# Kernel tuning notes

Hardware: AMD Instinct MI355X
Metric: run time of the kernel (lower is better)

## Reference

```python
import jax, jax.numpy as jnp
import numpy as np

N = 8192
FEAT = 3
TRIG = 2
SA = 2
H = 64
ACT = 3
NEG = -1.0e9
EPS = 1e-5


def setup_inputs() -> dict:
    key = jax.random.key(0)
    ks = jax.random.split(key, 24)
    s = 0.05
    node_features = jax.random.uniform(ks[0], (N, FEAT), dtype=jnp.float32)
    adj = jax.random.randint(ks[1], (N, N), 0, 2).astype(jnp.float32)
    # ensure self-loops so every row has at least one neighbor
    adj_matrix = jnp.maximum(adj, jnp.eye(N, dtype=jnp.float32))
    trigger_context = jax.random.uniform(ks[2], (TRIG,), dtype=jnp.float32)
    sa_priors = jax.random.normal(ks[3], (N, SA), dtype=jnp.float32)
    p = lambda k, sh: jax.random.normal(k, sh, dtype=jnp.float32) * s
    return {
        "node_features": node_features,
        "adj_matrix": adj_matrix,
        "trigger_context": trigger_context,
        "sa_priors": sa_priors,
        # node_encoder: Linear(5,64) -> ReLU -> Linear(64,64)
        "w1": p(ks[4], (FEAT + TRIG, H)), "b1": jnp.zeros((H,), jnp.float32),
        "w2": p(ks[5], (H, H)), "b2": jnp.zeros((H,), jnp.float32),
        "wq": p(ks[6], (H, H)), "bq": jnp.zeros((H,), jnp.float32),
        "wk": p(ks[7], (H, H)), "bk": jnp.zeros((H,), jnp.float32),
        "wg": p(ks[8], (TRIG, H)), "bg": jnp.zeros((H,), jnp.float32),
        "stateful_bias": jnp.zeros((1,), jnp.float32),
        "wm": p(ks[9], (H, H)), "bm": jnp.zeros((H,), jnp.float32),
        "ln_g": jnp.ones((H,), jnp.float32), "ln_b": jnp.zeros((H,), jnp.float32),
        "wa1": p(ks[10], (H + SA, H)), "ba1": jnp.zeros((H,), jnp.float32),
        "wa2": p(ks[11], (H, ACT)), "ba2": jnp.zeros((ACT,), jnp.float32),
    }


def reference(node_features, adj_matrix, trigger_context, sa_priors,
              w1, b1, w2, b2, wq, bq, wk, bk, wg, bg, stateful_bias,
              wm, bm, ln_g, ln_b, wa1, ba1, wa2, ba2):
    n = node_features.shape[0]
    trig = jnp.broadcast_to(trigger_context[None, :], (n, TRIG))
    x = jnp.concatenate([node_features, trig], axis=1)          # [N, 5]
    h = jax.nn.relu(x @ w1 + b1) @ w2 + b2                       # [N, H]
    q = h @ wq + bq
    k = h @ wk + bk
    scores = (q @ k.T) * (1.0 / np.sqrt(H))                      # [N, N]
    gate_factor = jnp.mean(jax.nn.sigmoid(trigger_context @ wg + bg))
    topo = jnp.where(adj_matrix == 0, jnp.float32(NEG), adj_matrix)
    is_stateful = node_features[:, 2]
    is_reactive = 1.0 - trigger_context[0]
    sb = jnp.outer(is_stateful, is_stateful) * (stateful_bias[0] * is_reactive)
    scores = scores * gate_factor + topo + sb
    attn = jax.nn.softmax(scores, axis=1)                        # [N, N]
    messages = h @ wm + bm
    aggregated = attn @ messages                                 # [N, H]
    z = h + aggregated
    mu = jnp.mean(z, axis=-1, keepdims=True)
    var = jnp.mean(jnp.square(z - mu), axis=-1, keepdims=True)
    emb = (z - mu) * jax.lax.rsqrt(var + EPS) * ln_g + ln_b      # LayerNorm
    ai = jnp.concatenate([emb, sa_priors], axis=1)               # [N, H+2]
    q_values = jax.nn.relu(ai @ wa1 + ba1) @ wa2 + ba2           # [N, 3]
    return q_values
```

## Files before the change

### kernel.cpp

```cpp
#include <hip/hip_runtime.h>
#include <hip/hip_bf16.h>
#include <math.h>

#define N 8192
#define NEGV -1000000000.0f
#define EPSV 1e-05f
#define NSPLIT 8
#define CPS (N / NSPLIT)
#define NTILE (CPS / 64)

typedef short bf16x8 __attribute__((ext_vector_type(8)));
typedef float f32x4 __attribute__((ext_vector_type(4)));
typedef unsigned short u16;

#define WS_SCAL 0
#define WS_H    64
#define WS_ST   (WS_H + N * 64)
#define WS_SBI  (WS_ST + N)
#define WS_DEN  (WS_SBI + N)
#define WS_AGG  (WS_DEN + NSPLIT * N)
#define WS_F_END (WS_AGG + NSPLIT * N * 64)
#define WU_BASE (WS_F_END * 2)
#define WU_QB (WU_BASE)
#define WU_KB (WU_BASE + N * 64)
#define WU_MB (WU_BASE + 2 * N * 64)
#define WU_MT (WU_BASE + 3 * N * 64)

static __device__ __forceinline__ u16 f2bf(float f) {
    __hip_bfloat16 h = __float2bfloat16(f);
    return *(u16*)&h;
}

__global__ void prep_k(const float* __restrict__ tc, const float* __restrict__ wg,
                       const float* __restrict__ bg, const float* __restrict__ sbias,
                       float* __restrict__ scal) {
    int j = threadIdx.x;
    float v = tc[0] * wg[j] + tc[1] * wg[64 + j] + bg[j];
    float g = 1.0f / (1.0f + __expf(-v));
    for (int off = 32; off; off >>= 1) g += __shfl_xor(g, off, 64);
    if (j == 0) {
        scal[0] = 0.125f * (g * (1.0f / 64.0f));
        scal[1] = sbias[0] * (1.0f - tc[0]);
    }
}

__global__ __launch_bounds__(256) void embed_k(
    const float* __restrict__ nf, const float* __restrict__ tc,
    const float* __restrict__ w1, const float* __restrict__ b1,
    const float* __restrict__ w2, const float* __restrict__ b2,
    const float* __restrict__ wq, const float* __restrict__ bq,
    const float* __restrict__ wk, const float* __restrict__ bk,
    const float* __restrict__ wm, const float* __restrict__ bm,
    float* __restrict__ ws)
{
    const int w = threadIdx.x >> 6, lane = threadIdx.x & 63;
    const int row = blockIdx.x * 4 + w;
    __shared__ float ts[4][64], hs[4][64];
    const float qscale = ws[WS_SCAL + 0];
    const float coef   = ws[WS_SCAL + 1];
    const float f0 = nf[row * 3], f1 = nf[row * 3 + 1], f2 = nf[row * 3 + 2];
    const float t0 = tc[0], t1 = tc[1];
    float v = b1[lane];
    v = fmaf(f0, w1[lane], v);
    v = fmaf(f1, w1[64 + lane], v);
    v = fmaf(f2, w1[128 + lane], v);
    v = fmaf(t0, w1[192 + lane], v);
    v = fmaf(t1, w1[256 + lane], v);
    ts[w][lane] = fmaxf(v, 0.0f);
    __syncthreads();
    float hv = b2[lane];
    #pragma unroll 8
    for (int j = 0; j < 64; j++) hv = fmaf(ts[w][j], w2[j * 64 + lane], hv);
    hs[w][lane] = hv;
    ws[WS_H + row * 64 + lane] = hv;
    __syncthreads();
    float qv = bq[lane], kv = bk[lane], mv = bm[lane];
    #pragma unroll 4
    for (int j = 0; j < 64; j++) {
        const float hj = hs[w][j];
        qv = fmaf(hj, wq[j * 64 + lane], qv);
        kv = fmaf(hj, wk[j * 64 + lane], kv);
        mv = fmaf(hj, wm[j * 64 + lane], mv);
    }
    u16* wu = (u16*)ws;
    wu[WU_QB + row * 64 + lane] = f2bf(qv * qscale);
    wu[WU_KB + row * 64 + lane] = f2bf(kv);
    wu[WU_MB + row * 64 + lane] = f2bf(mv);
    if (lane == 0) {
        ws[WS_ST + row]  = f2;
        ws[WS_SBI + row] = f2 * coef;
    }
}

__global__ __launch_bounds__(256) void transp_k(float* __restrict__ ws) {
    const u16* mb = (const u16*)ws + WU_MB;
    u16* mt = (u16*)ws + WU_MT;
    __shared__ __align__(16) u16 tile[64][72];
    const int i0 = blockIdx.x * 64;
    const int t = threadIdx.x;
    {
        const int r = t >> 2, cb = (t & 3) * 16;
        *(uint4*)&tile[r][cb]     = *(const uint4*)&mb[(size_t)(i0 + r) * 64 + cb];
        *(uint4*)&tile[r][cb + 8] = *(const uint4*)&mb[(size_t)(i0 + r) * 64 + cb + 8];
    }
    __syncthreads();
    const int c = t >> 2, rb = (t & 3) * 16;
    u16 tmp[16];
    #pragma unroll
    for (int i = 0; i < 16; i++) tmp[i] = tile[rb + i][c];
    *(uint4*)&mt[(size_t)c * N + i0 + rb]     = *(uint4*)&tmp[0];
    *(uint4*)&mt[(size_t)c * N + i0 + rb + 8] = *(uint4*)&tmp[8];
}

#define TILE_BODY(CUR, ADJ_RD, ST_RD, ADJ_WR, ST_WR)                          \
{                                                                             \
    const int jn = (jt + 64 < jend) ? (jt + 64) : jt;                         \
    _Pragma("unroll")                                                         \
    for (int reg = 0; reg < 4; reg++) {                                       \
        const size_t rowb = (size_t)(i0 + m0 + quad * 4 + reg) * N + jn + n16;\
        _Pragma("unroll")                                                     \
        for (int ct = 0; ct < 4; ct++) ADJ_WR[ct][reg] = adj[rowb + ct * 16]; \
    }                                                                         \
    _Pragma("unroll")                                                         \
    for (int ct = 0; ct < 4; ct++) ST_WR[ct] = st_g[jn + ct * 16 + n16];      \
    const uint4 kn0 = *(const uint4*)&kb[(size_t)(jn + sr) * 64 + scb];       \
    const uint4 kn1 = *(const uint4*)&kb[(size_t)(jn + sr) * 64 + scb + 8];   \
    const uint4 mn0 = *(const uint4*)&mt[(size_t)sr * N + jn + scb];          \
    const uint4 mn1 = *(const uint4*)&mt[(size_t)sr * N + jn + scb + 8];      \
    _Pragma("unroll")                                                         \
    for (int ct = 0; ct < 4; ct++) {                                          \
        const bf16x8 b0 = *(const bf16x8*)&ks[CUR][ct * 16 + n16][quad * 8];  \
        const bf16x8 b1 = *(const bf16x8*)&ks[CUR][ct * 16 + n16][32 + quad * 8]; \
        f32x4 s = {0.f, 0.f, 0.f, 0.f};                                       \
        s = __builtin_amdgcn_mfma_f32_16x16x32_bf16(aq0, b0, s, 0, 0, 0);     \
        s = __builtin_amdgcn_mfma_f32_16x16x32_bf16(aq1, b1, s, 0, 0, 0);     \
        const float stc = ST_RD[ct];                                          \
        _Pragma("unroll")                                                     \
        for (int reg = 0; reg < 4; reg++) {                                   \
            const float a = ADJ_RD[ct][reg];                                  \
            const float sc = s[reg] + (a == 0.0f ? NEGV : a) + sbr[reg] * stc;\
            const float p = __expf(sc);                                       \
            den[reg] += p;                                                    \
            ps[m0 + quad * 4 + reg][ct * 16 + n16] = f2bf(p);                 \
        }                                                                     \
    }                                                                         \
    __syncthreads();                                                          \
    {                                                                         \
        const bf16x8 ap0 = *(const bf16x8*)&ps[m0 + n16][quad * 8];           \
        const bf16x8 ap1 = *(const bf16x8*)&ps[m0 + n16][32 + quad * 8];      \
        _Pragma("unroll")                                                     \
        for (int nt = 0; nt < 4; nt++) {                                      \
            const bf16x8 b0 = *(const bf16x8*)&ms[CUR][nt * 16 + n16][quad * 8]; \
            const bf16x8 b1 = *(const bf16x8*)&ms[CUR][nt * 16 + n16][32 + quad * 8]; \
            acc[nt] = __builtin_amdgcn_mfma_f32_16x16x32_bf16(ap0, b0, acc[nt], 0, 0, 0); \
            acc[nt] = __builtin_amdgcn_mfma_f32_16x16x32_bf16(ap1, b1, acc[nt], 0, 0, 0); \
        }                                                                     \
    }                                                                         \
    *(uint4*)&ks[1 - (CUR)][sr][scb]     = kn0;                               \
    *(uint4*)&ks[1 - (CUR)][sr][scb + 8] = kn1;                               \
    *(uint4*)&ms[1 - (CUR)][sr][scb]     = mn0;                               \
    *(uint4*)&ms[1 - (CUR)][sr][scb + 8] = mn1;                               \
    __syncthreads();                                                          \
    jt += 64;                                                                 \
}

__global__ __launch_bounds__(256, 3) void attn_k(const float* __restrict__ adj,
                                                 float* __restrict__ ws)
{
    const int rb = blockIdx.x, sp = blockIdx.y;
    const int i0 = rb * 64, j0 = sp * CPS;
    const int jend = j0 + CPS;
    const int tid = threadIdx.x;
    const int lane = tid & 63;
    const int quad = lane >> 4, n16 = lane & 15;
    const int m0 = (tid >> 6) * 16;

    __shared__ __align__(16) u16 ks[2][64][72];
    __shared__ __align__(16) u16 ms[2][64][72];
    __shared__ __align__(16) u16 ps[64][76];

    const u16* qb = (const u16*)ws + WU_QB;
    const u16* kb = (const u16*)ws + WU_KB;
    const u16* mt = (const u16*)ws + WU_MT;
    const float* st_g = ws + WS_ST;

    const int sr = tid >> 2, scb = (tid & 3) * 16;

    float adjA[4][4], adjB[4][4], stA[4], stB[4];

    #pragma unroll
    for (int reg = 0; reg < 4; reg++) {
        const size_t rowb = (size_t)(i0 + m0 + quad * 4 + reg) * N + j0 + n16;
        #pragma unroll
        for (int ct = 0; ct < 4; ct++) adjA[ct][reg] = adj[rowb + ct * 16];
    }
    #pragma unroll
    for (int ct = 0; ct < 4; ct++) stA[ct] = st_g[j0 + ct * 16 + n16];
    {
        const uint4 k0 = *(const uint4*)&kb[(size_t)(j0 + sr) * 64 + scb];
        const uint4 k1 = *(const uint4*)&kb[(size_t)(j0 + sr) * 64 + scb + 8];
        const uint4 q0 = *(const uint4*)&mt[(size_t)sr * N + j0 + scb];
        const uint4 q1 = *(const uint4*)&mt[(size_t)sr * N + j0 + scb + 8];
        *(uint4*)&ks[0][sr][scb]     = k0;
        *(uint4*)&ks[0][sr][scb + 8] = k1;
        *(uint4*)&ms[0][sr][scb]     = q0;
        *(uint4*)&ms[0][sr][scb + 8] = q1;
    }

    const bf16x8 aq0 = *(const bf16x8*)&qb[(size_t)(i0 + m0 + n16) * 64 + quad * 8];
    const bf16x8 aq1 = *(const bf16x8*)&qb[(size_t)(i0 + m0 + n16) * 64 + 32 + quad * 8];
    float sbr[4];
    #pragma unroll
    for (int v = 0; v < 4; v++) sbr[v] = ws[WS_SBI + i0 + m0 + quad * 4 + v];

    f32x4 acc[4];
    #pragma unroll
    for (int i = 0; i < 4; i++) acc[i] = (f32x4){0.f, 0.f, 0.f, 0.f};
    float den[4] = {0.f, 0.f, 0.f, 0.f};

    __syncthreads();

    int jt = j0;
    for (int t = 0; t < NTILE; t += 2) {
        TILE_BODY(0, adjA, stA, adjB, stB)
        TILE_BODY(1, adjB, stB, adjA, stA)
    }

    float* aggp = ws + WS_AGG + (size_t)sp * N * 64;
    #pragma unroll
    for (int nt = 0; nt < 4; nt++) {
        #pragma unroll
        for (int reg = 0; reg < 4; reg++) {
            aggp[(size_t)(i0 + m0 + quad * 4 + reg) * 64 + nt * 16 + n16] = acc[nt][reg];
        }
    }
    #pragma unroll
    for (int reg = 0; reg < 4; reg++) {
        float d = den[reg];
        d += __shfl_xor(d, 1, 64);
        d += __shfl_xor(d, 2, 64);
        d += __shfl_xor(d, 4, 64);
        d += __shfl_xor(d, 8, 64);
        if (n16 == 0) ws[WS_DEN + sp * N + i0 + m0 + quad * 4 + reg] = d;
    }
}

__global__ __launch_bounds__(256) void final_k(
    const float* __restrict__ sa, const float* __restrict__ ln_g,
    const float* __restrict__ ln_b,
    const float* __restrict__ wa1, const float* __restrict__ ba1,
    const float* __restrict__ wa2, const float* __restrict__ ba2,
    const float* __restrict__ ws, float* __restrict__ out)
{
    const int w = threadIdx.x >> 6, lane = threadIdx.x & 63;
    const int row = blockIdx.x * 4 + w;
    __shared__ float es[4][64], hs2[4][64];
    float a = 0.0f;
    #pragma unroll
    for (int sp = 0; sp < NSPLIT; sp++)
        a += ws[WS_AGG + (size_t)sp * N * 64 + (size_t)row * 64 + lane];
    float d = 0.0f;
    #pragma unroll
    for (int sp = 0; sp < NSPLIT; sp++) d += ws[WS_DEN + sp * N + row];
    const float z = ws[WS_H + row * 64 + lane] + a / d;
    float mu = z;
    for (int off = 32; off; off >>= 1) mu += __shfl_xor(mu, off, 64);
    mu *= (1.0f / 64.0f);
    const float zc = z - mu;
    float var = zc * zc;
    for (int off = 32; off; off >>= 1) var += __shfl_xor(var, off, 64);
    var *= (1.0f / 64.0f);
    const float emb = zc * rsqrtf(var + EPSV) * ln_g[lane] + ln_b[lane];
    es[w][lane] = emb;
    __syncthreads();
    const float sa0 = sa[row * 2], sa1 = sa[row * 2 + 1];
    float hv = ba1[lane];
    #pragma unroll 8
    for (int c = 0; c < 64; c++) hv = fmaf(es[w][c], wa1[c * 64 + lane], hv);
    hv = fmaf(sa0, wa1[64 * 64 + lane], hv);
    hv = fmaf(sa1, wa1[65 * 64 + lane], hv);
    hs2[w][lane] = fmaxf(hv, 0.0f);
    __syncthreads();
    if (lane < 3) {
        float o = ba2[lane];
        for (int u = 0; u < 64; u++) o = fmaf(hs2[w][u], wa2[u * 3 + lane], o);
        out[row * 3 + lane] = o;
    }
}

extern "C" void kernel_launch(void* const* d_in, const int* in_sizes, int n_in,
                              void* d_out, int out_size, void* d_ws, size_t ws_size,
                              hipStream_t stream)
{
    const float* nf  = (const float*)d_in[0];
    const float* adj = (const float*)d_in[1];
    const float* tc  = (const float*)d_in[2];
    const float* sa  = (const float*)d_in[3];
    const float* w1  = (const float*)d_in[4];
    const float* b1  = (const float*)d_in[5];
    const float* w2  = (const float*)d_in[6];
    const float* b2  = (const float*)d_in[7];
    const float* wq  = (const float*)d_in[8];
    const float* bq  = (const float*)d_in[9];
    const float* wk  = (const float*)d_in[10];
    const float* bk  = (const float*)d_in[11];
    const float* wg  = (const float*)d_in[12];
    const float* bg  = (const float*)d_in[13];
    const float* sb  = (const float*)d_in[14];
    const float* wm  = (const float*)d_in[15];
    const float* bm  = (const float*)d_in[16];
    const float* lng = (const float*)d_in[17];
    const float* lnb = (const float*)d_in[18];
    const float* wa1 = (const float*)d_in[19];
    const float* ba1 = (const float*)d_in[20];
    const float* wa2 = (const float*)d_in[21];
    const float* ba2 = (const float*)d_in[22];
    float* ws  = (float*)d_ws;
    float* out = (float*)d_out;

    prep_k<<<1, 64, 0, stream>>>(tc, wg, bg, sb, ws + WS_SCAL);
    embed_k<<<N / 4, 256, 0, stream>>>(nf, tc, w1, b1, w2, b2, wq, bq, wk, bk,
                                       wm, bm, ws);
    transp_k<<<N / 64, 256, 0, stream>>>(ws);
    attn_k<<<dim3(N / 64, NSPLIT), 256, 0, stream>>>(adj, ws);
    final_k<<<N / 4, 256, 0, stream>>>(sa, lng, lnb, wa1, ba1, wa2, ba2, ws, out);
}
```

Baseline: 491.6 us.

## Vectorize adjacency loads via column permutation and deepen K/M prefetch to two tiles

The key tile rows are loaded in a permuted order (psr), so each lane owns four consecutive score columns. The adjacency and stateful-bias reads then become float4 loads, and the probabilities are written to shared memory as ushort4. The K and message tile prefetch now runs two tiles ahead through rotating register sets instead of one, so global latency gets more time to be hidden. This aims to cut the number of global load instructions and scalar LDS stores in the softmax-weighted attention loop, at the cost of more live registers under a 3-block occupancy target.

```diff
diff --git a/kernel.cpp b/kernel.cpp
--- a/kernel.cpp
+++ b/kernel.cpp
@@ -112,39 +112,64 @@
     *(uint4*)&mt[(size_t)c * N + i0 + rb + 8] = *(uint4*)&tmp[8];
 }
 
-#define TILE_BODY(CUR, ADJ_RD, ST_RD, ADJ_WR, ST_WR)                          \
+#define TILE_BODY(CUR, KL, KS_, ADJ, ST)                                      \
 {                                                                             \
-    const int jn = (jt + 64 < jend) ? (jt + 64) : jt;                         \
-    _Pragma("unroll")                                                         \
-    for (int reg = 0; reg < 4; reg++) {                                       \
-        const size_t rowb = (size_t)(i0 + m0 + quad * 4 + reg) * N + jn + n16;\
-        _Pragma("unroll")                                                     \
-        for (int ct = 0; ct < 4; ct++) ADJ_WR[ct][reg] = adj[rowb + ct * 16]; \
-    }                                                                         \
-    _Pragma("unroll")                                                         \
-    for (int ct = 0; ct < 4; ct++) ST_WR[ct] = st_g[jn + ct * 16 + n16];      \
-    const uint4 kn0 = *(const uint4*)&kb[(size_t)(jn + sr) * 64 + scb];       \
-    const uint4 kn1 = *(const uint4*)&kb[(size_t)(jn + sr) * 64 + scb + 8];   \
-    const uint4 mn0 = *(const uint4*)&mt[(size_t)sr * N + jn + scb];          \
-    const uint4 mn1 = *(const uint4*)&mt[(size_t)sr * N + jn + scb + 8];      \
+                           \
+    const int jk = (jt + 128 < jend) ? (jt + 128) : (jend - 64);              \
+    KL##0 = *(const uint4*)&kb[(size_t)(jk + psr) * 64 + scb];                \
+    KL##1 = *(const uint4*)&kb[(size_t)(jk + psr) * 64 + scb + 8];            \
+    KL##2 = *(const uint4*)&mt[(size_t)sr * N + jk + scb];                    \
+    KL##3 = *(const uint4*)&mt[(size_t)sr * N + jk + scb + 8];                \
+                             \
+    f32x4 s[4];                                                               \
     _Pragma("unroll")                                                         \
     for (int ct = 0; ct < 4; ct++) {                                          \
         const bf16x8 b0 = *(const bf16x8*)&ks[CUR][ct * 16 + n16][quad * 8];  \
         const bf16x8 b1 = *(const bf16x8*)&ks[CUR][ct * 16 + n16][32 + quad * 8]; \
-        f32x4 s = {0.f, 0.f, 0.f, 0.f};                                       \
-        s = __builtin_amdgcn_mfma_f32_16x16x32_bf16(aq0, b0, s, 0, 0, 0);     \
-        s = __builtin_amdgcn_mfma_f32_16x16x32_bf16(aq1, b1, s, 0, 0, 0);     \
-        const float stc = ST_RD[ct];                                          \
+        f32x4 sv = {0.f, 0.f, 0.f, 0.f};                                      \
+        sv = __builtin_amdgcn_mfma_f32_16x16x32_bf16(aq0, b0, sv, 0, 0, 0);   \
+        sv = __builtin_amdgcn_mfma_f32_16x16x32_bf16(aq1, b1, sv, 0, 0, 0);   \
+        s[ct] = sv;                                                           \
+    }                                                                         \
+             \
+    _Pragma("unroll")                                                         \
+    for (int reg = 0; reg < 4; reg++) {                                       \
+        ushort4 pw;                                                           \
+        float p0, p1, p2, p3;                                                 \
+        {                                                                     \
+            const float a = ADJ[reg][0];                                      \
+            p0 = __expf(s[0][reg] + (a == 0.0f ? NEGV : a) + sbr[reg] * ST[0]); \
+        }                                                                     \
+        {                                                                     \
+            const float a = ADJ[reg][1];                                      \
+            p1 = __expf(s[1][reg] + (a == 0.0f ? NEGV : a) + sbr[reg] * ST[1]); \
+        }                                                                     \
+        {                                                                     \
+            const float a = ADJ[reg][2];                                      \
+            p2 = __expf(s[2][reg] + (a == 0.0f ? NEGV : a) + sbr[reg] * ST[2]); \
+        }                                                                     \
+        {                                                                     \
+            const float a = ADJ[reg][3];                                      \
+            p3 = __expf(s[3][reg] + (a == 0.0f ? NEGV : a) + sbr[reg] * ST[3]); \
+        }                                                                     \
+        den[reg] += (p0 + p1) + (p2 + p3);                                    \
+        pw.x = f2bf(p0); pw.y = f2bf(p1); pw.z = f2bf(p2); pw.w = f2bf(p3);   \
+        *(ushort4*)&ps[m0 + quad * 4 + reg][n16 * 4] = pw;                    \
+    }                                                                         \
+    \
+    {                                                                         \
+        const int ja = (jt + 128 < jend) ? (jt + 128) : (jend - 64);          \
         _Pragma("unroll")                                                     \
         for (int reg = 0; reg < 4; reg++) {                                   \
-            const float a = ADJ_RD[ct][reg];                                  \
-            const float sc = s[reg] + (a == 0.0f ? NEGV : a) + sbr[reg] * stc;\
-            const float p = __expf(sc);                                       \
-            den[reg] += p;                                                    \
-            ps[m0 + quad * 4 + reg][ct * 16 + n16] = f2bf(p);                 \
-        }                                                                     \
+            const float4 a4 = *(const float4*)&adj[(size_t)(i0 + m0 + quad * 4 + reg) * N + ja + n16 * 4]; \
+            ADJ[reg][0] = a4.x; ADJ[reg][1] = a4.y;                           \
+            ADJ[reg][2] = a4.z; ADJ[reg][3] = a4.w;                           \
+        }                                                                     \
+        const float4 s4 = *(const float4*)&st_g[ja + n16 * 4];                \
+        ST[0] = s4.x; ST[1] = s4.y; ST[2] = s4.z; ST[3] = s4.w;               \
     }                                                                         \
     __syncthreads();                                                          \
+                                          \
     {                                                                         \
         const bf16x8 ap0 = *(const bf16x8*)&ps[m0 + n16][quad * 8];           \
         const bf16x8 ap1 = *(const bf16x8*)&ps[m0 + n16][32 + quad * 8];      \
@@ -156,10 +181,11 @@
             acc[nt] = __builtin_amdgcn_mfma_f32_16x16x32_bf16(ap1, b1, acc[nt], 0, 0, 0); \
         }                                                                     \
     }                                                                         \
-    *(uint4*)&ks[1 - (CUR)][sr][scb]     = kn0;                               \
-    *(uint4*)&ks[1 - (CUR)][sr][scb + 8] = kn1;                               \
-    *(uint4*)&ms[1 - (CUR)][sr][scb]     = mn0;                               \
-    *(uint4*)&ms[1 - (CUR)][sr][scb + 8] = mn1;                               \
+           \
+    *(uint4*)&ks[1 - (CUR)][sr][scb]     = KS_##0;                            \
+    *(uint4*)&ks[1 - (CUR)][sr][scb + 8] = KS_##1;                            \
+    *(uint4*)&ms[1 - (CUR)][sr][scb]     = KS_##2;                            \
+    *(uint4*)&ms[1 - (CUR)][sr][scb + 8] = KS_##3;                            \
     __syncthreads();                                                          \
     jt += 64;                                                                 \
 }
@@ -185,27 +211,40 @@
     const float* st_g = ws + WS_ST;
 
     const int sr = tid >> 2, scb = (tid & 3) * 16;
-
+    const int psr = ((sr & 15) << 2) | (sr >> 4);
+
+    uint4 kmA0, kmA1, kmA2, kmA3, kmB0, kmB1, kmB2, kmB3;
     float adjA[4][4], adjB[4][4], stA[4], stB[4];
 
-    #pragma unroll
-    for (int reg = 0; reg < 4; reg++) {
-        const size_t rowb = (size_t)(i0 + m0 + quad * 4 + reg) * N + j0 + n16;
-        #pragma unroll
-        for (int ct = 0; ct < 4; ct++) adjA[ct][reg] = adj[rowb + ct * 16];
-    }
-    #pragma unroll
-    for (int ct = 0; ct < 4; ct++) stA[ct] = st_g[j0 + ct * 16 + n16];
     {
-        const uint4 k0 = *(const uint4*)&kb[(size_t)(j0 + sr) * 64 + scb];
-        const uint4 k1 = *(const uint4*)&kb[(size_t)(j0 + sr) * 64 + scb + 8];
+        const uint4 k0 = *(const uint4*)&kb[(size_t)(j0 + psr) * 64 + scb];
+        const uint4 k1 = *(const uint4*)&kb[(size_t)(j0 + psr) * 64 + scb + 8];
         const uint4 q0 = *(const uint4*)&mt[(size_t)sr * N + j0 + scb];
         const uint4 q1 = *(const uint4*)&mt[(size_t)sr * N + j0 + scb + 8];
+        const int j1 = j0 + 64;
+        kmB0 = *(const uint4*)&kb[(size_t)(j1 + psr) * 64 + scb];
+        kmB1 = *(const uint4*)&kb[(size_t)(j1 + psr) * 64 + scb + 8];
+        kmB2 = *(const uint4*)&mt[(size_t)sr * N + j1 + scb];
+        kmB3 = *(const uint4*)&mt[(size_t)sr * N + j1 + scb + 8];
         *(uint4*)&ks[0][sr][scb]     = k0;
         *(uint4*)&ks[0][sr][scb + 8] = k1;
         *(uint4*)&ms[0][sr][scb]     = q0;
         *(uint4*)&ms[0][sr][scb + 8] = q1;
     }
+    #pragma unroll
+    for (int reg = 0; reg < 4; reg++) {
+        const size_t rowb = (size_t)(i0 + m0 + quad * 4 + reg) * N + n16 * 4;
+        const float4 a0 = *(const float4*)&adj[rowb + j0];
+        adjA[reg][0] = a0.x; adjA[reg][1] = a0.y; adjA[reg][2] = a0.z; adjA[reg][3] = a0.w;
+        const float4 a1 = *(const float4*)&adj[rowb + j0 + 64];
+        adjB[reg][0] = a1.x; adjB[reg][1] = a1.y; adjB[reg][2] = a1.z; adjB[reg][3] = a1.w;
+    }
+    {
+        const float4 s0 = *(const float4*)&st_g[j0 + n16 * 4];
+        stA[0] = s0.x; stA[1] = s0.y; stA[2] = s0.z; stA[3] = s0.w;
+        const float4 s1 = *(const float4*)&st_g[j0 + 64 + n16 * 4];
+        stB[0] = s1.x; stB[1] = s1.y; stB[2] = s1.z; stB[3] = s1.w;
+    }
 
     const bf16x8 aq0 = *(const bf16x8*)&qb[(size_t)(i0 + m0 + n16) * 64 + quad * 8];
     const bf16x8 aq1 = *(const bf16x8*)&qb[(size_t)(i0 + m0 + n16) * 64 + 32 + quad * 8];
@@ -222,8 +261,8 @@
 
     int jt = j0;
     for (int t = 0; t < NTILE; t += 2) {
-        TILE_BODY(0, adjA, stA, adjB, stB)
-        TILE_BODY(1, adjB, stB, adjA, stA)
+        TILE_BODY(0, kmA, kmB, adjA, stA)
+        TILE_BODY(1, kmB, kmA, adjB, stB)
     }
 
     float* aggp = ws + WS_AGG + (size_t)sp * N * 64;
```

Result: slower. 524.0 us (+6.6%).
